# Kernel optimization log

Hardware: AMD Instinct MI355X
Metric: run time of the kernel (lower is better)

## Reference

```python
import jax, jax.numpy as jnp
import numpy as np

IN_FEATURES = 4096
OUT_FEATURES = 4096
N_TOKENS = 8192


def setup_inputs() -> dict:
    key = jax.random.key(0)
    kx, kw = jax.random.split(key)
    x = jax.random.normal(kx, (N_TOKENS, IN_FEATURES), dtype=jnp.float32)
    # weight = randn(out, in) * 0.1, bias = zeros(out), per BinaryLinear.__init__
    weight = jax.random.normal(kw, (OUT_FEATURES, IN_FEATURES), dtype=jnp.float32) * 0.1
    bias = jnp.zeros((OUT_FEATURES,), dtype=jnp.float32)
    return {"x": x, "weight": weight, "bias": bias}


def reference(x, weight, bias):
    # sign-binarize weights (torch .sign(): -1/0/+1, matched by jnp.sign),
    # then dense linear: x @ sign(W)^T + b
    bin_w = jnp.sign(weight)
    return jnp.einsum('ni,oi->no', x, bin_w) + bias
```

## Files before the change

kernel.cpp:

```cpp
#include <hip/hip_runtime.h>
#include <stdint.h>

typedef __attribute__((ext_vector_type(4)))  int i32x4;
typedef __attribute__((ext_vector_type(16))) int i32x16;

#define M_TOK 8192
#define N_OUT 4096
#define K_IN  4096

#define BM 256
#define BN 256
#define BKB 64
#define NT (K_IN / BKB)
#define SLOT_BYTES 32768
#define B_OFF 16384

#define GLDS16(gp, lp)                                                         \
  __builtin_amdgcn_global_load_lds(                                            \
      (const __attribute__((address_space(1))) void*)(gp),                     \
      (__attribute__((address_space(3))) void*)(lp), 16, 0, 0)

#define VM4 asm volatile("s_waitcnt vmcnt(4)" ::: "memory")
#define VM8 asm volatile("s_waitcnt vmcnt(8)" ::: "memory")
#define VM0 asm volatile("s_waitcnt vmcnt(0)" ::: "memory")
#define SB0 __builtin_amdgcn_sched_barrier(0)
#define NOPX ((void)0)

__global__ void __launch_bounds__(256) quant_fused(
    const float* __restrict__ x, const float* __restrict__ w,
    char* __restrict__ xq, char* __restrict__ wq, float* __restrict__ scales) {
  __shared__ float wmax[4];
  const int t = threadIdx.x;

  if (blockIdx.x < M_TOK) {
    const int row = blockIdx.x;
    const float4* rp = (const float4*)(x + (size_t)row * K_IN);

    float4 v[4];
#pragma unroll
    for (int p = 0; p < 4; p++) v[p] = rp[p * 256 + t];

    float amax = 0.f;
#pragma unroll
    for (int p = 0; p < 4; p++)
      amax = fmaxf(amax, fmaxf(fmaxf(fabsf(v[p].x), fabsf(v[p].y)),
                               fmaxf(fabsf(v[p].z), fabsf(v[p].w))));

#pragma unroll
    for (int off = 32; off > 0; off >>= 1)
      amax = fmaxf(amax, __shfl_xor(amax, off));

    if ((t & 63) == 0) wmax[t >> 6] = amax;
    __syncthreads();
    amax = fmaxf(fmaxf(wmax[0], wmax[1]), fmaxf(wmax[2], wmax[3]));
    amax = fmaxf(amax, 1e-30f);

    const float inv = 127.f / amax;
    if (t == 0) scales[row] = amax / 127.f;

    uint32_t* op = (uint32_t*)(xq + (size_t)row * K_IN);
#pragma unroll
    for (int p = 0; p < 4; p++) {
      uint32_t b0 = (uint32_t)(__float2int_rn(v[p].x * inv) & 0xFF);
      uint32_t b1 = (uint32_t)(__float2int_rn(v[p].y * inv) & 0xFF);
      uint32_t b2 = (uint32_t)(__float2int_rn(v[p].z * inv) & 0xFF);
      uint32_t b3 = (uint32_t)(__float2int_rn(v[p].w * inv) & 0xFF);
      op[p * 256 + t] = b0 | (b1 << 8) | (b2 << 16) | (b3 << 24);
    }
  } else {
    const size_t base = (size_t)(blockIdx.x - M_TOK) * 1024;
    const float4* p = (const float4*)w + base;
    uint32_t* op = (uint32_t*)wq + base;
#pragma unroll
    for (int q = 0; q < 4; q++) {
      float4 f = p[q * 256 + t];
      int s0 = (f.x > 0.f) - (f.x < 0.f);
      int s1 = (f.y > 0.f) - (f.y < 0.f);
      int s2 = (f.z > 0.f) - (f.z < 0.f);
      int s3 = (f.w > 0.f) - (f.w < 0.f);
      op[q * 256 + t] = (uint32_t)(s0 & 0xFF) | ((uint32_t)(s1 & 0xFF) << 8) |
                        ((uint32_t)(s2 & 0xFF) << 16) | ((uint32_t)(s3 & 0xFF) << 24);
    }
  }
}

struct Frags {
  i32x4 a[2][4];
  i32x4 b[2][2];
};

__global__ void __launch_bounds__(512, 2) gemm_bin_i8(
    const char* __restrict__ A, const char* __restrict__ B,
    const float* __restrict__ scales, const float* __restrict__ bias,
    float* __restrict__ C) {
  __shared__ __align__(16) char lds[4 * SLOT_BYTES];

  const int tid  = threadIdx.x;
  const int lane = tid & 63;
  const int wv   = tid >> 6;
  const int wm   = wv >> 2;
  const int wn   = wv & 3;

  int bid = (int)blockIdx.x;
  bid = (bid & 7) * (512 >> 3) + (bid >> 3);
  const int m0 = (bid >> 4) * BM;
  const int n0 = (bid & 15) * BN;

  const int srow   = lane >> 2;
  const int schunk = (lane & 3) ^ ((lane >> 3) & 3);
  const char* gAb = A + (size_t)(m0 + wv * 32 + srow) * K_IN + schunk * 16;
  const char* gBb = B + (size_t)(n0 + wv * 32 + srow) * K_IN + schunk * 16;
  char* lAb = lds + wv * 2048;
  char* lBb = lds + B_OFF + wv * 2048;

  auto stage = [&](int tt) {
    const size_t ko = (size_t)tt * BKB;
    char* la = lAb + (tt & 3) * SLOT_BYTES;
    char* lb = lBb + (tt & 3) * SLOT_BYTES;
    GLDS16(gAb + ko, la);
    GLDS16(gAb + ko + (size_t)16 * K_IN, la + 1024);
    GLDS16(gBb + ko, lb);
    GLDS16(gBb + ko + (size_t)16 * K_IN, lb + 1024);
  };

  const int fr  = lane & 31;
  const int k16 = lane >> 5;
  const int x3  = (lane >> 1) & 3;
  const int aoff = wm * 8192 + fr * 64;
  const int boff = B_OFF + wn * 4096 + fr * 64;
  const int so0 = ((0 + k16) ^ x3) << 4;
  const int so1 = ((2 + k16) ^ x3) << 4;

  i32x16 acc[4][2];
#pragma unroll
  for (int m = 0; m < 4; m++)
#pragma unroll
    for (int n = 0; n < 2; n++)
#pragma unroll
      for (int r = 0; r < 16; r++) acc[m][n][r] = 0;

  Frags f0, f1;

#define READF(f, tt)                                                           \
  {                                                                            \
    const char* pA_ = lds + ((tt) & 3) * SLOT_BYTES + aoff;                    \
    const char* pB_ = lds + ((tt) & 3) * SLOT_BYTES + boff;                    \
    f.a[0][0] = *(const i32x4*)(pA_ + so0);                                    \
    f.a[0][1] = *(const i32x4*)(pA_ + 2048 + so0);                             \
    f.a[0][2] = *(const i32x4*)(pA_ + 4096 + so0);                             \
    f.a[0][3] = *(const i32x4*)(pA_ + 6144 + so0);                             \
    f.b[0][0] = *(const i32x4*)(pB_ + so0);                                    \
    f.b[0][1] = *(const i32x4*)(pB_ + 2048 + so0);                             \
    f.a[1][0] = *(const i32x4*)(pA_ + so1);                                    \
    f.a[1][1] = *(const i32x4*)(pA_ + 2048 + so1);                             \
    f.a[1][2] = *(const i32x4*)(pA_ + 4096 + so1);                             \
    f.a[1][3] = *(const i32x4*)(pA_ + 6144 + so1);                             \
    f.b[1][0] = *(const i32x4*)(pB_ + so1);                                    \
    f.b[1][1] = *(const i32x4*)(pB_ + 2048 + so1);                             \
  }

#define MFMAF(f)                                                               \
  {                                                                            \
    __builtin_amdgcn_s_setprio(1);                                             \
    acc[0][0] = __builtin_amdgcn_mfma_i32_32x32x32_i8(f.a[0][0], f.b[0][0], acc[0][0], 0, 0, 0); \
    acc[0][1] = __builtin_amdgcn_mfma_i32_32x32x32_i8(f.a[0][0], f.b[0][1], acc[0][1], 0, 0, 0); \
    acc[1][0] = __builtin_amdgcn_mfma_i32_32x32x32_i8(f.a[0][1], f.b[0][0], acc[1][0], 0, 0, 0); \
    acc[1][1] = __builtin_amdgcn_mfma_i32_32x32x32_i8(f.a[0][1], f.b[0][1], acc[1][1], 0, 0, 0); \
    acc[2][0] = __builtin_amdgcn_mfma_i32_32x32x32_i8(f.a[0][2], f.b[0][0], acc[2][0], 0, 0, 0); \
    acc[2][1] = __builtin_amdgcn_mfma_i32_32x32x32_i8(f.a[0][2], f.b[0][1], acc[2][1], 0, 0, 0); \
    acc[3][0] = __builtin_amdgcn_mfma_i32_32x32x32_i8(f.a[0][3], f.b[0][0], acc[3][0], 0, 0, 0); \
    acc[3][1] = __builtin_amdgcn_mfma_i32_32x32x32_i8(f.a[0][3], f.b[0][1], acc[3][1], 0, 0, 0); \
    acc[0][0] = __builtin_amdgcn_mfma_i32_32x32x32_i8(f.a[1][0], f.b[1][0], acc[0][0], 0, 0, 0); \
    acc[0][1] = __builtin_amdgcn_mfma_i32_32x32x32_i8(f.a[1][0], f.b[1][1], acc[0][1], 0, 0, 0); \
    acc[1][0] = __builtin_amdgcn_mfma_i32_32x32x32_i8(f.a[1][1], f.b[1][0], acc[1][0], 0, 0, 0); \
    acc[1][1] = __builtin_amdgcn_mfma_i32_32x32x32_i8(f.a[1][1], f.b[1][1], acc[1][1], 0, 0, 0); \
    acc[2][0] = __builtin_amdgcn_mfma_i32_32x32x32_i8(f.a[1][2], f.b[1][0], acc[2][0], 0, 0, 0); \
    acc[2][1] = __builtin_amdgcn_mfma_i32_32x32x32_i8(f.a[1][2], f.b[1][1], acc[2][1], 0, 0, 0); \
    acc[3][0] = __builtin_amdgcn_mfma_i32_32x32x32_i8(f.a[1][3], f.b[1][0], acc[3][0], 0, 0, 0); \
    acc[3][1] = __builtin_amdgcn_mfma_i32_32x32x32_i8(f.a[1][3], f.b[1][1], acc[3][1], 0, 0, 0); \
    __builtin_amdgcn_s_setprio(0);                                             \
  }

#define ITER(t_, fc, fn, STAGE_STMT, VM_STMT)                                  \
  {                                                                            \
    VM_STMT;                                                                   \
    SB0;                                                                       \
    __builtin_amdgcn_s_barrier();                                              \
    SB0;                                                                       \
    STAGE_STMT;                                                                \
    READF(fn, (t_) + 1);                                                       \
    MFMAF(fc);                                                                 \
  }

  stage(0); stage(1); stage(2);
  VM8;
  SB0;
  __builtin_amdgcn_s_barrier();
  SB0;
  READF(f0, 0);

  for (int I = 0; I < 30; ++I) {
    const int t0 = 2 * I;
    ITER(t0,     f0, f1, stage(t0 + 3), VM4);
    ITER(t0 + 1, f1, f0, stage(t0 + 4), VM4);
  }
  ITER(60, f0, f1, stage(63), VM4);
  ITER(61, f1, f0, NOPX, VM4);
  ITER(62, f0, f1, NOPX, VM0);
  MFMAF(f1);
#undef ITER
#undef MFMAF
#undef READF

  const int col0 = n0 + wn * 64 + (lane & 31);
  const float bv0 = bias[col0];
  const float bv1 = bias[col0 + 32];
#pragma unroll
  for (int m = 0; m < 4; m++) {
    const int rb = m0 + wm * 128 + m * 32 + ((lane >> 5) << 2);
#pragma unroll
    for (int r = 0; r < 16; r++) {
      const int row = rb + (r & 3) + ((r >> 2) << 3);
      const float sc = scales[row];
      float* cp = C + (size_t)row * N_OUT + col0;
      cp[0]  = (float)acc[m][0][r] * sc + bv0;
      cp[32] = (float)acc[m][1][r] * sc + bv1;
    }
  }
}

__global__ void fallback_gemm(const float* __restrict__ x, const float* __restrict__ w,
                              const float* __restrict__ bias, float* __restrict__ out) {
  int idx = blockIdx.x * blockDim.x + threadIdx.x;
  if (idx >= M_TOK * N_OUT) return;
  int row = idx / N_OUT, col = idx % N_OUT;
  const float* xp = x + (size_t)row * K_IN;
  const float* wp = w + (size_t)col * K_IN;
  float s = 0.f;
  for (int k = 0; k < K_IN; k++) {
    float wv = wp[k];
    float sg = wv > 0.f ? 1.f : (wv < 0.f ? -1.f : 0.f);
    s += xp[k] * sg;
  }
  out[idx] = s + bias[col];
}

extern "C" void kernel_launch(void* const* d_in, const int* in_sizes, int n_in,
                              void* d_out, int out_size, void* d_ws, size_t ws_size,
                              hipStream_t stream) {
  const float* x    = (const float*)d_in[0];
  const float* w    = (const float*)d_in[1];
  const float* bias = (const float*)d_in[2];
  float* out = (float*)d_out;

  const size_t xq_bytes = (size_t)M_TOK * K_IN;
  const size_t wq_bytes = (size_t)N_OUT * K_IN;
  const size_t sc_bytes = (size_t)M_TOK * sizeof(float);

  if (ws_size < xq_bytes + wq_bytes + sc_bytes) {
    int total = M_TOK * N_OUT;
    fallback_gemm<<<(total + 255) / 256, 256, 0, stream>>>(x, w, bias, out);
    return;
  }

  char*  xq = (char*)d_ws;
  char*  wq = (char*)d_ws + xq_bytes;
  float* sc = (float*)((char*)d_ws + xq_bytes + wq_bytes);

  quant_fused<<<M_TOK + (N_OUT * K_IN / 4) / 1024, 256, 0, stream>>>(x, w, xq, wq, sc);

  gemm_bin_i8<<<512, 512, 0, stream>>>(xq, wq, sc, bias, out);
}
```

Baseline: 397.3 us.

## Use four waves per block with 128x128 per-wave tiles in int8 GEMM

Halves the threads per GEMM block from 512 to 256, so each wave computes a 128x128 output tile (4x4 MFMA accumulators) instead of 128x64. Each wave now issues twice as many global-to-LDS loads per stage, and the vmcnt waits are raised to match. The aim is more register-level reuse of the A/B fragments per LDS read and fewer waves contending for the block barrier. In exchange the accumulators double to 256 VGPRs per lane and occupancy drops to one block per CU with fewer waves to hide latency.

```diff
diff --git a/kernel.cpp b/kernel.cpp
--- a/kernel.cpp
+++ b/kernel.cpp
@@ -20,10 +20,10 @@
       (const __attribute__((address_space(1))) void*)(gp),                     \
       (__attribute__((address_space(3))) void*)(lp), 16, 0, 0)
 
-#define VM4 asm volatile("s_waitcnt vmcnt(4)" ::: "memory")
-#define VM8 asm volatile("s_waitcnt vmcnt(8)" ::: "memory")
-#define VM0 asm volatile("s_waitcnt vmcnt(0)" ::: "memory")
-#define SB0 __builtin_amdgcn_sched_barrier(0)
+#define VM16 asm volatile("s_waitcnt vmcnt(16)" ::: "memory")
+#define VM8  asm volatile("s_waitcnt vmcnt(8)" ::: "memory")
+#define VM0  asm volatile("s_waitcnt vmcnt(0)" ::: "memory")
+#define SB0  __builtin_amdgcn_sched_barrier(0)
 #define NOPX ((void)0)
 
 __global__ void __launch_bounds__(256) quant_fused(
@@ -86,10 +86,10 @@
 
 struct Frags {
   i32x4 a[2][4];
-  i32x4 b[2][2];
+  i32x4 b[2][4];
 };
 
-__global__ void __launch_bounds__(512, 2) gemm_bin_i8(
+__global__ void __launch_bounds__(256, 1) gemm_bin_i8(
     const char* __restrict__ A, const char* __restrict__ B,
     const float* __restrict__ scales, const float* __restrict__ bias,
     float* __restrict__ C) {
@@ -98,8 +98,8 @@
   const int tid  = threadIdx.x;
   const int lane = tid & 63;
   const int wv   = tid >> 6;
-  const int wm   = wv >> 2;
-  const int wn   = wv & 3;
+  const int wm   = wv >> 1;
+  const int wn   = wv & 1;
 
   int bid = (int)blockIdx.x;
   bid = (bid & 7) * (512 >> 3) + (bid >> 3);
@@ -108,34 +108,36 @@
 
   const int srow   = lane >> 2;
   const int schunk = (lane & 3) ^ ((lane >> 3) & 3);
-  const char* gAb = A + (size_t)(m0 + wv * 32 + srow) * K_IN + schunk * 16;
-  const char* gBb = B + (size_t)(n0 + wv * 32 + srow) * K_IN + schunk * 16;
-  char* lAb = lds + wv * 2048;
-  char* lBb = lds + B_OFF + wv * 2048;
+  const char* gAb = A + (size_t)(m0 + wv * 64 + srow) * K_IN + schunk * 16;
+  const char* gBb = B + (size_t)(n0 + wv * 64 + srow) * K_IN + schunk * 16;
+  char* lAb = lds + wv * 4096;
+  char* lBb = lds + B_OFF + wv * 4096;
 
   auto stage = [&](int tt) {
     const size_t ko = (size_t)tt * BKB;
     char* la = lAb + (tt & 3) * SLOT_BYTES;
     char* lb = lBb + (tt & 3) * SLOT_BYTES;
-    GLDS16(gAb + ko, la);
-    GLDS16(gAb + ko + (size_t)16 * K_IN, la + 1024);
-    GLDS16(gBb + ko, lb);
-    GLDS16(gBb + ko + (size_t)16 * K_IN, lb + 1024);
+#pragma unroll
+    for (int g = 0; g < 4; g++)
+      GLDS16(gAb + ko + (size_t)(g * 16) * K_IN, la + g * 1024);
+#pragma unroll
+    for (int g = 0; g < 4; g++)
+      GLDS16(gBb + ko + (size_t)(g * 16) * K_IN, lb + g * 1024);
   };
 
   const int fr  = lane & 31;
   const int k16 = lane >> 5;
   const int x3  = (lane >> 1) & 3;
   const int aoff = wm * 8192 + fr * 64;
-  const int boff = B_OFF + wn * 4096 + fr * 64;
+  const int boff = B_OFF + wn * 8192 + fr * 64;
   const int so0 = ((0 + k16) ^ x3) << 4;
   const int so1 = ((2 + k16) ^ x3) << 4;
 
-  i32x16 acc[4][2];
+  i32x16 acc[4][4];
 #pragma unroll
   for (int m = 0; m < 4; m++)
 #pragma unroll
-    for (int n = 0; n < 2; n++)
+    for (int n = 0; n < 4; n++)
 #pragma unroll
       for (int r = 0; r < 16; r++) acc[m][n][r] = 0;
 
@@ -151,33 +153,43 @@
     f.a[0][3] = *(const i32x4*)(pA_ + 6144 + so0);                             \
     f.b[0][0] = *(const i32x4*)(pB_ + so0);                                    \
     f.b[0][1] = *(const i32x4*)(pB_ + 2048 + so0);                             \
+    f.b[0][2] = *(const i32x4*)(pB_ + 4096 + so0);                             \
+    f.b[0][3] = *(const i32x4*)(pB_ + 6144 + so0);                             \
     f.a[1][0] = *(const i32x4*)(pA_ + so1);                                    \
     f.a[1][1] = *(const i32x4*)(pA_ + 2048 + so1);                             \
     f.a[1][2] = *(const i32x4*)(pA_ + 4096 + so1);                             \
     f.a[1][3] = *(const i32x4*)(pA_ + 6144 + so1);                             \
     f.b[1][0] = *(const i32x4*)(pB_ + so1);                                    \
     f.b[1][1] = *(const i32x4*)(pB_ + 2048 + so1);                             \
+    f.b[1][2] = *(const i32x4*)(pB_ + 4096 + so1);                             \
+    f.b[1][3] = *(const i32x4*)(pB_ + 6144 + so1);                             \
+  }
+
+#define MFMA1(ks, f)                                                           \
+  {                                                                            \
+    acc[0][0] = __builtin_amdgcn_mfma_i32_32x32x32_i8(f.a[ks][0], f.b[ks][0], acc[0][0], 0, 0, 0); \
+    acc[0][1] = __builtin_amdgcn_mfma_i32_32x32x32_i8(f.a[ks][0], f.b[ks][1], acc[0][1], 0, 0, 0); \
+    acc[0][2] = __builtin_amdgcn_mfma_i32_32x32x32_i8(f.a[ks][0], f.b[ks][2], acc[0][2], 0, 0, 0); \
+    acc[0][3] = __builtin_amdgcn_mfma_i32_32x32x32_i8(f.a[ks][0], f.b[ks][3], acc[0][3], 0, 0, 0); \
+    acc[1][0] = __builtin_amdgcn_mfma_i32_32x32x32_i8(f.a[ks][1], f.b[ks][0], acc[1][0], 0, 0, 0); \
+    acc[1][1] = __builtin_amdgcn_mfma_i32_32x32x32_i8(f.a[ks][1], f.b[ks][1], acc[1][1], 0, 0, 0); \
+    acc[1][2] = __builtin_amdgcn_mfma_i32_32x32x32_i8(f.a[ks][1], f.b[ks][2], acc[1][2], 0, 0, 0); \
+    acc[1][3] = __builtin_amdgcn_mfma_i32_32x32x32_i8(f.a[ks][1], f.b[ks][3], acc[1][3], 0, 0, 0); \
+    acc[2][0] = __builtin_amdgcn_mfma_i32_32x32x32_i8(f.a[ks][2], f.b[ks][0], acc[2][0], 0, 0, 0); \
+    acc[2][1] = __builtin_amdgcn_mfma_i32_32x32x32_i8(f.a[ks][2], f.b[ks][1], acc[2][1], 0, 0, 0); \
+    acc[2][2] = __builtin_amdgcn_mfma_i32_32x32x32_i8(f.a[ks][2], f.b[ks][2], acc[2][2], 0, 0, 0); \
+    acc[2][3] = __builtin_amdgcn_mfma_i32_32x32x32_i8(f.a[ks][2], f.b[ks][3], acc[2][3], 0, 0, 0); \
+    acc[3][0] = __builtin_amdgcn_mfma_i32_32x32x32_i8(f.a[ks][3], f.b[ks][0], acc[3][0], 0, 0, 0); \
+    acc[3][1] = __builtin_amdgcn_mfma_i32_32x32x32_i8(f.a[ks][3], f.b[ks][1], acc[3][1], 0, 0, 0); \
+    acc[3][2] = __builtin_amdgcn_mfma_i32_32x32x32_i8(f.a[ks][3], f.b[ks][2], acc[3][2], 0, 0, 0); \
+    acc[3][3] = __builtin_amdgcn_mfma_i32_32x32x32_i8(f.a[ks][3], f.b[ks][3], acc[3][3], 0, 0, 0); \
   }
 
 #define MFMAF(f)                                                               \
   {                                                                            \
     __builtin_amdgcn_s_setprio(1);                                             \
-    acc[0][0] = __builtin_amdgcn_mfma_i32_32x32x32_i8(f.a[0][0], f.b[0][0], acc[0][0], 0, 0, 0); \
-    acc[0][1] = __builtin_amdgcn_mfma_i32_32x32x32_i8(f.a[0][0], f.b[0][1], acc[0][1], 0, 0, 0); \
-    acc[1][0] = __builtin_amdgcn_mfma_i32_32x32x32_i8(f.a[0][1], f.b[0][0], acc[1][0], 0, 0, 0); \
-    acc[1][1] = __builtin_amdgcn_mfma_i32_32x32x32_i8(f.a[0][1], f.b[0][1], acc[1][1], 0, 0, 0); \
-    acc[2][0] = __builtin_amdgcn_mfma_i32_32x32x32_i8(f.a[0][2], f.b[0][0], acc[2][0], 0, 0, 0); \
-    acc[2][1] = __builtin_amdgcn_mfma_i32_32x32x32_i8(f.a[0][2], f.b[0][1], acc[2][1], 0, 0, 0); \
-    acc[3][0] = __builtin_amdgcn_mfma_i32_32x32x32_i8(f.a[0][3], f.b[0][0], acc[3][0], 0, 0, 0); \
-    acc[3][1] = __builtin_amdgcn_mfma_i32_32x32x32_i8(f.a[0][3], f.b[0][1], acc[3][1], 0, 0, 0); \
-    acc[0][0] = __builtin_amdgcn_mfma_i32_32x32x32_i8(f.a[1][0], f.b[1][0], acc[0][0], 0, 0, 0); \
-    acc[0][1] = __builtin_amdgcn_mfma_i32_32x32x32_i8(f.a[1][0], f.b[1][1], acc[0][1], 0, 0, 0); \
-    acc[1][0] = __builtin_amdgcn_mfma_i32_32x32x32_i8(f.a[1][1], f.b[1][0], acc[1][0], 0, 0, 0); \
-    acc[1][1] = __builtin_amdgcn_mfma_i32_32x32x32_i8(f.a[1][1], f.b[1][1], acc[1][1], 0, 0, 0); \
-    acc[2][0] = __builtin_amdgcn_mfma_i32_32x32x32_i8(f.a[1][2], f.b[1][0], acc[2][0], 0, 0, 0); \
-    acc[2][1] = __builtin_amdgcn_mfma_i32_32x32x32_i8(f.a[1][2], f.b[1][1], acc[2][1], 0, 0, 0); \
-    acc[3][0] = __builtin_amdgcn_mfma_i32_32x32x32_i8(f.a[1][3], f.b[1][0], acc[3][0], 0, 0, 0); \
-    acc[3][1] = __builtin_amdgcn_mfma_i32_32x32x32_i8(f.a[1][3], f.b[1][1], acc[3][1], 0, 0, 0); \
+    MFMA1(0, f);                                                               \
+    MFMA1(1, f);                                                               \
     __builtin_amdgcn_s_setprio(0);                                             \
   }
 
@@ -193,7 +205,7 @@
   }
 
   stage(0); stage(1); stage(2);
-  VM8;
+  VM16;
   SB0;
   __builtin_amdgcn_s_barrier();
   SB0;
@@ -201,20 +213,22 @@
 
   for (int I = 0; I < 30; ++I) {
     const int t0 = 2 * I;
-    ITER(t0,     f0, f1, stage(t0 + 3), VM4);
-    ITER(t0 + 1, f1, f0, stage(t0 + 4), VM4);
-  }
-  ITER(60, f0, f1, stage(63), VM4);
-  ITER(61, f1, f0, NOPX, VM4);
+    ITER(t0,     f0, f1, stage(t0 + 3), VM8);
+    ITER(t0 + 1, f1, f0, stage(t0 + 4), VM8);
+  }
+  ITER(60, f0, f1, stage(63), VM8);
+  ITER(61, f1, f0, NOPX, VM8);
   ITER(62, f0, f1, NOPX, VM0);
   MFMAF(f1);
 #undef ITER
 #undef MFMAF
+#undef MFMA1
 #undef READF
 
-  const int col0 = n0 + wn * 64 + (lane & 31);
-  const float bv0 = bias[col0];
-  const float bv1 = bias[col0 + 32];
+  const int col0 = n0 + wn * 128 + (lane & 31);
+  float bv[4];
+#pragma unroll
+  for (int n = 0; n < 4; n++) bv[n] = bias[col0 + n * 32];
 #pragma unroll
   for (int m = 0; m < 4; m++) {
     const int rb = m0 + wm * 128 + m * 32 + ((lane >> 5) << 2);
@@ -223,8 +237,10 @@
       const int row = rb + (r & 3) + ((r >> 2) << 3);
       const float sc = scales[row];
       float* cp = C + (size_t)row * N_OUT + col0;
-      cp[0]  = (float)acc[m][0][r] * sc + bv0;
-      cp[32] = (float)acc[m][1][r] * sc + bv1;
+      cp[0]  = (float)acc[m][0][r] * sc + bv[0];
+      cp[32] = (float)acc[m][1][r] * sc + bv[1];
+      cp[64] = (float)acc[m][2][r] * sc + bv[2];
+      cp[96] = (float)acc[m][3][r] * sc + bv[3];
     }
   }
 }
@@ -269,5 +285,5 @@
 
   quant_fused<<<M_TOK + (N_OUT * K_IN / 4) / 1024, 256, 0, stream>>>(x, w, xq, wq, sc);
 
-  gemm_bin_i8<<<512, 512, 0, stream>>>(xq, wq, sc, bias, out);
-}
+  gemm_bin_i8<<<512, 256, 0, stream>>>(xq, wq, sc, bias, out);
+}
```

Measured after the change: 403.6 us. About the same (+1.6%).
